# Kernel optimization log

Measured on AMD Instinct MI355X. Metric: run time of the kernel, lower is better.

The kernel has to match this reference:

```python
import jax, jax.numpy as jnp
import numpy as np

B, S, D, H = 2, 2048, 1024, 16
HD = D // H  # head dim = 64


def setup_inputs() -> dict:
    key = jax.random.key(0)
    k0, k1, k2 = jax.random.split(key, 3)
    x = jax.random.normal(k0, (B, S, D), dtype=jnp.float32)
    # fused QKV projection: nn.Linear(D, 3D) -> weight [3D, D], bias [3D]
    Wqkv_w = jax.random.normal(k1, (3 * D, D), dtype=jnp.float32) * (1.0 / np.sqrt(D))
    Wqkv_b = jnp.zeros((3 * D,), dtype=jnp.float32)
    out_w = jax.random.normal(k2, (D, D), dtype=jnp.float32) * (1.0 / np.sqrt(D))
    out_b = jnp.zeros((D,), dtype=jnp.float32)
    # ALiBi-like additive bias, shape [1, H, 1, S] (broadcasts over queries)
    slopes = 2.0 ** (-8.0 * jnp.arange(1, H + 1, dtype=jnp.float32) / H)  # [H]
    dist = (S - 1) - jnp.arange(S, dtype=jnp.float32)                      # [S]
    attn_bias = (-slopes[:, None] * dist[None, :]).reshape(1, H, 1, S)
    # key padding mask: second sequence is padded by 256 tokens at the end
    lengths = jnp.array([S, S - 256])
    attention_mask = jnp.arange(S)[None, :] < lengths[:, None]             # [B, S] bool
    return {"x": x, "Wqkv_w": Wqkv_w, "Wqkv_b": Wqkv_b, "out_w": out_w,
            "out_b": out_b, "attn_bias": attn_bias, "attention_mask": attention_mask}


def reference(x, Wqkv_w, Wqkv_b, out_w, out_b, attn_bias, attention_mask):
    b, s, d = x.shape
    # fused QKV projection, then chunk into q, k, v along feature dim
    qkv = jnp.einsum('bsd,ed->bse', x, Wqkv_w) + Wqkv_b  # [b, s, 3d]
    q, k, v = jnp.split(qkv, 3, axis=-1)
    # b s (h hd) -> b h s hd
    q = q.reshape(b, s, H, HD).transpose(0, 2, 1, 3)
    k = k.reshape(b, s, H, HD).transpose(0, 2, 1, 3)
    v = v.reshape(b, s, H, HD).transpose(0, 2, 1, 3)
    softmax_scale = 1.0 / np.sqrt(HD)
    aw = jnp.einsum('bhqe,bhke->bhqk', q, k) * softmax_scale  # [b, H, s, s]
    aw = aw + attn_bias  # attn_bias broadcasts [1,H,1,s] -> [b,H,s,s]
    min_val = jnp.finfo(aw.dtype).min
    # key padding mask: mask positions where attention_mask is False
    aw = jnp.where(attention_mask[:, None, None, :], aw, min_val)
    # causal mask (is_causal=True, s_q == s_k)
    causal = jnp.tril(jnp.ones((s, s), dtype=bool))
    aw = jnp.where(causal[None, None, :, :], aw, min_val)
    p = jax.nn.softmax(aw, axis=-1)
    out = jnp.einsum('bhqk,bhke->bhqe', p, v)  # [b, H, s, HD]
    out = out.transpose(0, 2, 1, 3).reshape(b, s, d)
    return jnp.einsum('bsd,ed->bse', out, out_w) + out_b
```

## Files before the change

kernel.cpp:

```cpp
#include <hip/hip_runtime.h>
#include <hip/hip_bf16.h>
#include <stdint.h>

typedef __attribute__((ext_vector_type(8))) short s16x8;
typedef __attribute__((ext_vector_type(8))) unsigned short u16x8;
typedef __attribute__((ext_vector_type(4))) float f32x4;

#define SEQ 2048
#define LOG2E 1.44269504088896f

__device__ __forceinline__ unsigned short f2b(float x) {
  union { __hip_bfloat16 h; unsigned short u; } cv;
  cv.h = __float2bfloat16(x);
  return cv.u;
}

__device__ __forceinline__ float exp2fast(float x) {
  float r;
  asm("v_exp_f32 %0, %1" : "=v"(r) : "v"(x));
  return r;
}

__device__ __forceinline__ void gload16(const void* g, void* l) {
  __builtin_amdgcn_global_load_lds(
      (const __attribute__((address_space(1))) void*)g,
      (__attribute__((address_space(3))) void*)l, 16, 0, 0);
}

__global__ void cvt_all(const float* __restrict__ x, const float* __restrict__ wq,
                        const float* __restrict__ ow, const float* __restrict__ abias,
                        const void* __restrict__ maskp,
                        __hip_bfloat16* __restrict__ xb, __hip_bfloat16* __restrict__ wqb,
                        __hip_bfloat16* __restrict__ owb, float* __restrict__ biasm) {
  const int i = blockIdx.x * 256 + threadIdx.x;
  if (i >= 2097152) {
    const int j = i - 2097152;
    const int b = j >> 15, h = (j >> 11) & 15, kv = j & 2047;
    const int* mi = (const int*)maskp;
    const unsigned char* mb = (const unsigned char*)maskp;
    const bool int_fmt = (mi[0] == 0 || mi[0] == 1);
    const bool ok = int_fmt ? (mi[b * SEQ + kv] != 0) : (mb[b * SEQ + kv] != 0);
    biasm[j] = ok ? abias[h * SEQ + kv] * LOG2E : -1e30f;
    return;
  }
  const float* src;
  __hip_bfloat16* dst;
  int off;
  if (i < 1048576) { src = x; dst = xb; off = i; }
  else if (i < 1835008) { src = wq; dst = wqb; off = i - 1048576; }
  else { src = ow; dst = owb; off = i - 1835008; }
  float4 v = reinterpret_cast<const float4*>(src)[off];
  ushort4 o;
  o.x = f2b(v.x); o.y = f2b(v.y); o.z = f2b(v.z); o.w = f2b(v.w);
  const int offs = off ^ ((((unsigned)off >> 8) & 3) << 1);
  reinterpret_cast<ushort4*>(dst)[offs] = o;
}

template <int MODE, int BM>
__global__ __launch_bounds__(256) void gemm_bt(
    const __hip_bfloat16* __restrict__ A, const __hip_bfloat16* __restrict__ B,
    const float* __restrict__ bias, void* __restrict__ Cout,
    __hip_bfloat16* __restrict__ Vt, int M, int N, int K) {
  constexpr int MR = BM / 32;
  __shared__ __align__(16) __hip_bfloat16 As[2][BM * 32];
  __shared__ __align__(16) __hip_bfloat16 Bs[2][128 * 32];
  const int tid = threadIdx.x;
  const int lane = tid & 63;
  const int w = tid >> 6;
  const int wr = w >> 1, wc = w & 1;
  const int rowg = blockIdx.x * BM;
  const int colg = blockIdx.y * 128;
  const int lr = lane & 15;
  const int lk = (((lane >> 4) ^ (lr & 3)) * 8);
  f32x4 acc[MR][4];
#pragma unroll
  for (int m = 0; m < MR; ++m)
#pragma unroll
    for (int n = 0; n < 4; ++n) acc[m][n] = (f32x4){0.f, 0.f, 0.f, 0.f};
#define GSTAGE(KT, C)                                                            \
  {                                                                              \
    _Pragma("unroll") for (int r = 0; r < BM / 64; ++r) {                        \
      const int idx = r * 256 + tid;                                             \
      gload16(A + (size_t)(rowg + (idx >> 2)) * K + (KT) + (idx & 3) * 8,        \
              &As[C][0] + idx * 8);                                              \
    }                                                                            \
    _Pragma("unroll") for (int r = 0; r < 2; ++r) {                              \
      const int idx = r * 256 + tid;                                             \
      gload16(B + (size_t)(colg + (idx >> 2)) * K + (KT) + (idx & 3) * 8,        \
              &Bs[C][0] + idx * 8);                                              \
    }                                                                            \
  }
  GSTAGE(0, 0);
  __syncthreads();
  int cur = 0;
  for (int kt = 0; kt < K; kt += 32) {
    if (kt + 32 < K) GSTAGE(kt + 32, cur ^ 1);
    s16x8 af[MR], bfr[4];
#pragma unroll
    for (int m = 0; m < MR; ++m)
      af[m] = *reinterpret_cast<const s16x8*>(&As[cur][0] +
                                              (wr * (BM / 2) + m * 16 + lr) * 32 + lk);
#pragma unroll
    for (int n = 0; n < 4; ++n)
      bfr[n] = *reinterpret_cast<const s16x8*>(&Bs[cur][0] +
                                               (wc * 64 + n * 16 + lr) * 32 + lk);
#pragma unroll
    for (int m = 0; m < MR; ++m)
#pragma unroll
      for (int n = 0; n < 4; ++n)
        acc[m][n] = __builtin_amdgcn_mfma_f32_16x16x32_bf16(af[m], bfr[n], acc[m][n], 0, 0, 0);
    __syncthreads();
    cur ^= 1;
  }
#undef GSTAGE
  const int r0l = (lane >> 4) * 4;
  float bvn[4];
#pragma unroll
  for (int n = 0; n < 4; ++n) bvn[n] = bias[colg + wc * 64 + n * 16 + lr];
#pragma unroll
  for (int m = 0; m < MR; ++m) {
#pragma unroll
    for (int n = 0; n < 4; ++n) {
      const int col = colg + wc * 64 + n * 16 + lr;
      const int row0 = rowg + wr * (BM / 2) + m * 16 + r0l;
      const float bv = bvn[n];
      if (MODE == 0) {
        __hip_bfloat16* qkb = (__hip_bfloat16*)Cout;
        if (col < 1024) {
#pragma unroll
          for (int j = 0; j < 4; ++j)
            qkb[(size_t)(row0 + j) * 2048 + col] = __float2bfloat16(acc[m][n][j] + bv);
        } else if (col < 2048) {
          const int dd = col & 63;
          const int base = col - dd;
#pragma unroll
          for (int j = 0; j < 4; ++j) {
            const int s = row0 + j;
            qkb[(size_t)s * 2048 + base + (dd ^ ((s & 7) << 3))] =
                __float2bfloat16(acc[m][n][j] + bv);
          }
        } else {
          const int c2 = col - 2048;
          const int dd = c2 & 63;
          const int bb = row0 >> 11;
          const int s0 = (row0 & 2047) ^ ((dd & 7) << 3);
          ushort4 pk;
          unsigned short* pp = (unsigned short*)&pk;
#pragma unroll
          for (int j = 0; j < 4; ++j) pp[j] = f2b(acc[m][n][j] + bv);
          *reinterpret_cast<ushort4*>(
              Vt + ((size_t)(bb * 16 + (c2 >> 6)) * 64 + dd) * 2048 + s0) = pk;
        }
      } else {
        float* o = (float*)Cout;
#pragma unroll
        for (int j = 0; j < 4; ++j)
          o[(size_t)(row0 + j) * N + col] = acc[m][n][j] + bv;
      }
    }
  }
}

__device__ __forceinline__ void attn_tile(
    const char* Ks, const char* Vs, char* pw, const float* bmb,
    s16x8 aq0, s16x8 aq1, int lane, int kv0, int q_abs, bool causal,
    int rd0, int rd1, const int* pwo,
    float m_r, float& l_r, f32x4* oa) {
  const int g = lane >> 4;
  const float SCALE2 = 0.125f * LOG2E;
  f32x4 bvp[4];
#pragma unroll
  for (int n = 0; n < 4; ++n) {
    bvp[n] = *reinterpret_cast<const f32x4*>(bmb + kv0 + n * 16 + g * 4);
#pragma unroll
    for (int j = 0; j < 4; ++j) bvp[n][j] -= m_r;
  }
  f32x4 sf[4];
  __builtin_amdgcn_s_setprio(1);
#pragma unroll
  for (int n = 0; n < 4; ++n) {
    s16x8 ak0 = *reinterpret_cast<const s16x8*>(Ks + rd0 + n * 2048);
    s16x8 ak1 = *reinterpret_cast<const s16x8*>(Ks + rd1 + n * 2048);
    f32x4 z = (f32x4){0.f, 0.f, 0.f, 0.f};
    z = __builtin_amdgcn_mfma_f32_16x16x32_bf16(ak0, aq0, z, 0, 0, 0);
    z = __builtin_amdgcn_mfma_f32_16x16x32_bf16(ak1, aq1, z, 0, 0, 0);
    sf[n] = z;
  }
  __builtin_amdgcn_s_setprio(0);
#pragma unroll
  for (int n = 0; n < 4; ++n)
#pragma unroll
    for (int j = 0; j < 4; ++j) sf[n][j] = fmaf(sf[n][j], SCALE2, bvp[n][j]);
  if (causal) {
    const int kvb = kv0 + g * 4;
#pragma unroll
    for (int n = 0; n < 4; ++n)
#pragma unroll
      for (int j = 0; j < 4; ++j)
        if (kvb + n * 16 + j > q_abs) sf[n][j] = -1e30f;
  }
  float ps[4];
#pragma unroll
  for (int n = 0; n < 4; ++n) {
#pragma unroll
    for (int j = 0; j < 4; ++j) sf[n][j] = exp2fast(sf[n][j]);
    ps[n] = (sf[n][0] + sf[n][1]) + (sf[n][2] + sf[n][3]);
  }
  l_r += (ps[0] + ps[1]) + (ps[2] + ps[3]);
  s16x8 bva[4], bvb[4];
#pragma unroll
  for (int d = 0; d < 4; ++d) {
    bva[d] = *reinterpret_cast<const s16x8*>(Vs + rd0 + d * 2048);
    bvb[d] = *reinterpret_cast<const s16x8*>(Vs + rd1 + d * 2048);
  }
#pragma unroll
  for (int n = 0; n < 4; ++n) {
    union { ushort4 u; uint2 v; } pk;
    pk.u.x = f2b(sf[n][0]); pk.u.y = f2b(sf[n][1]);
    pk.u.z = f2b(sf[n][2]); pk.u.w = f2b(sf[n][3]);
    *reinterpret_cast<uint2*>(pw + pwo[n]) = pk.v;
  }
  s16x8 pa0 = *reinterpret_cast<const s16x8*>(pw + rd0);
  s16x8 pa1 = *reinterpret_cast<const s16x8*>(pw + rd1);
  __builtin_amdgcn_s_setprio(1);
#pragma unroll
  for (int d = 0; d < 4; ++d) {
    oa[d] = __builtin_amdgcn_mfma_f32_16x16x32_bf16(pa0, bva[d], oa[d], 0, 0, 0);
    oa[d] = __builtin_amdgcn_mfma_f32_16x16x32_bf16(pa1, bvb[d], oa[d], 0, 0, 0);
  }
  __builtin_amdgcn_s_setprio(0);
}

__global__ __launch_bounds__(512, 4) void attn_fwd6(
    const __hip_bfloat16* __restrict__ qk, const __hip_bfloat16* __restrict__ Vt,
    const float* __restrict__ biasm, __hip_bfloat16* __restrict__ O) {
  __shared__ __align__(16) char KV[2][2][2][8192];
  __shared__ __align__(16) char Ps[8][2048];
  const int tid = threadIdx.x;
  const int lane = tid & 63;
  const int w = tid >> 6;
  const int wsub = w & 3;
  const int z = w >> 2;
  const int bid = blockIdx.x;
  const int qt = 31 - (bid >> 5);
  const int bh = bid & 31;
  const int b = bh >> 4, h = bh & 15;
  const int row0 = qt * 64 + wsub * 16;
  const int lr = lane & 15;
  const int g = lane >> 4;
  const int NTit = (qt >> 1) + 1;
  const int xm = (lr & 7) << 4;
  const int lkB = g * 16;
  const int rd0 = lr * 128 + (lkB ^ xm);
  const int rd1 = lr * 128 + ((64 + lkB) ^ xm);
  const int pwo[4] = {lr * 128 + ((g * 8) ^ xm),       lr * 128 + ((32 + g * 8) ^ xm),
                      lr * 128 + ((64 + g * 8) ^ xm),  lr * 128 + ((96 + g * 8) ^ xm)};
  const __hip_bfloat16* qptr =
      qk + (size_t)(b * SEQ + row0 + lr) * 2048 + h * 64 + g * 8;
  const s16x8 aq0 = *reinterpret_cast<const s16x8*>(qptr);
  const s16x8 aq1 = *reinterpret_cast<const s16x8*>(qptr + 32);
  const int q_abs = row0 + lr;
  const float* bmb = biasm + (size_t)bh * 2048;
  float mb = bmb[q_abs];
  if (mb < -1e29f) {
    int lo = 0, hi = q_abs;
    while (lo < hi) {
      const int mid = (lo + hi + 1) >> 1;
      if (bmb[mid] < -1e29f) hi = mid - 1; else lo = mid;
    }
    mb = bmb[lo];
  }
  const float m_r = mb + 12.0f;
  float l_r = 0.f;
  f32x4 oa[4];
#pragma unroll
  for (int d = 0; d < 4; ++d) oa[d] = (f32x4){0.f, 0.f, 0.f, 0.f};
  const int r_ = tid >> 3;
  const int c16 = tid & 7;
  const __hip_bfloat16* kb = qk + ((size_t)b * SEQ + r_) * 2048 + 1024 + h * 64 + c16 * 8;
  const __hip_bfloat16* vb = Vt + ((size_t)bh * 64 + r_) * 2048 + c16 * 8;
#define ISSUE(T, C)                                                     \
  {                                                                     \
    const int tE_ = 2 * (T);                                            \
    const int tO_ = (2 * (T) + 1 <= qt) ? (2 * (T) + 1) : qt;           \
    gload16(kb + (size_t)(tE_ * 64) * 2048, KV[0][C][0] + tid * 16);    \
    gload16(kb + (size_t)(tO_ * 64) * 2048, KV[1][C][0] + tid * 16);    \
    gload16(vb + tE_ * 64, KV[0][C][1] + tid * 16);                     \
    gload16(vb + tO_ * 64, KV[1][C][1] + tid * 16);                     \
  }
  ISSUE(0, 0);
  __syncthreads();
  int cur = 0;
  for (int t = 0; t < NTit; ++t) {
    if (t + 1 < NTit) ISSUE(t + 1, cur ^ 1);
    const int tz = 2 * t + z;
    if (tz <= qt)
      attn_tile(KV[z][cur][0], KV[z][cur][1], Ps[w], bmb, aq0, aq1, lane,
                tz * 64, q_abs, tz == qt, rd0, rd1, pwo, m_r, l_r, oa);
    __syncthreads();
    cur ^= 1;
  }
#undef ISSUE
  l_r += __shfl_xor(l_r, 16);
  l_r += __shfl_xor(l_r, 32);
  float* mlbuf = (float*)&KV[0][0][0][0];
  if (z == 1) {
    float* mo = (float*)(&Ps[0][0] + wsub * 4096);
#pragma unroll
    for (int d = 0; d < 4; ++d)
#pragma unroll
      for (int j = 0; j < 4; ++j)
        mo[(g * 4 + j) * 64 + d * 16 + lr] = oa[d][j];
    if (lane < 16) {
      mlbuf[wsub * 32 + lr] = m_r;
      mlbuf[wsub * 32 + 16 + lr] = l_r;
    }
  }
  __syncthreads();
  if (z == 0) {
    const float mB = mlbuf[wsub * 32 + lr];
    const float lB = mlbuf[wsub * 32 + 16 + lr];
    const float mS = fmaxf(m_r, mB);
    const float fA = exp2fast(m_r - mS);
    const float fB = exp2fast(mB - mS);
    const float linv = 1.0f / (l_r * fA + lB * fB);
    float fAj[4], fBj[4], lij[4];
#pragma unroll
    for (int j = 0; j < 4; ++j) {
      fAj[j] = __shfl(fA, g * 4 + j);
      fBj[j] = __shfl(fB, g * 4 + j);
      lij[j] = __shfl(linv, g * 4 + j);
    }
    const float* mo = (const float*)(&Ps[0][0] + wsub * 4096);
#pragma unroll
    for (int d = 0; d < 4; ++d)
#pragma unroll
      for (int j = 0; j < 4; ++j) {
        const float v =
            (oa[d][j] * fAj[j] + mo[(g * 4 + j) * 64 + d * 16 + lr] * fBj[j]) * lij[j];
        O[(size_t)(b * SEQ + row0 + g * 4 + j) * 1024 +
          ((h * 64 + d * 16 + lr) ^ (j << 3))] = __float2bfloat16(v);
      }
  }
}

extern "C" void kernel_launch(void* const* d_in, const int* in_sizes, int n_in,
                              void* d_out, int out_size, void* d_ws, size_t ws_size,
                              hipStream_t stream) {
  const float* x     = (const float*)d_in[0];
  const float* wqkv  = (const float*)d_in[1];
  const float* bqkv  = (const float*)d_in[2];
  const float* wout  = (const float*)d_in[3];
  const float* bout  = (const float*)d_in[4];
  const float* abias = (const float*)d_in[5];
  const void*  mask  = d_in[6];

  __hip_bfloat16* ws  = (__hip_bfloat16*)d_ws;
  __hip_bfloat16* xb  = ws;
  __hip_bfloat16* wqb = ws + 4194304;
  __hip_bfloat16* owb = ws + 7340032;
  __hip_bfloat16* qkb = ws + 8388608;
  __hip_bfloat16* vtb = ws + 16777216;
  float*          bmf = (float*)(ws + 20971520);
  __hip_bfloat16* aob = xb;

  cvt_all<<<8448, 256, 0, stream>>>(x, wqkv, wout, abias, mask, xb, wqb, owb, bmf);
  gemm_bt<0, 128><<<dim3(32, 24), 256, 0, stream>>>(xb, wqb, bqkv, (void*)qkb, vtb,
                                                    4096, 3072, 1024);
  attn_fwd6<<<1024, 512, 0, stream>>>(qkb, vtb, bmf, aob);
  gemm_bt<1, 64><<<dim3(64, 8), 256, 0, stream>>>(aob, owb, bout, d_out,
                                                  (__hip_bfloat16*)nullptr, 4096, 1024, 1024);
}
```

Baseline: 107.2 us.

## Keep softmax probabilities in registers by permuting K rows to match MFMA layout

Permutes which K rows each lane reads, and the matching bias and causal-mask indices, so the QK^T MFMA output already sits in the A-operand layout of the PV MFMA. The probabilities are then packed with v_cvt_pk_bf16_f32 straight into registers instead of going through an LDS write and read-back. This removes the per-wave Ps shared buffer, which lowers LDS use and may raise occupancy. The K swizzle in the QKV projection epilogue is changed to match the new read pattern, and the merge scratch now reuses the KV buffer, which needs care to avoid correctness or bank-conflict problems.

```diff
diff --git a/kernel.cpp b/kernel.cpp
--- a/kernel.cpp
+++ b/kernel.cpp
@@ -18,6 +18,12 @@
 __device__ __forceinline__ float exp2fast(float x) {
   float r;
   asm("v_exp_f32 %0, %1" : "=v"(r) : "v"(x));
+  return r;
+}
+
+__device__ __forceinline__ unsigned int cvtpk(float lo, float hi) {
+  unsigned int r;
+  asm("v_cvt_pk_bf16_f32 %0, %1, %2" : "=v"(r) : "v"(lo), "v"(hi));
   return r;
 }
 
@@ -136,7 +142,8 @@
 #pragma unroll
           for (int j = 0; j < 4; ++j) {
             const int s = row0 + j;
-            qkb[(size_t)s * 2048 + base + (dd ^ ((s & 7) << 3))] =
+            const int fs = (s & 3) | ((s & 8) >> 1);
+            qkb[(size_t)s * 2048 + base + (dd ^ (fs << 3))] =
                 __float2bfloat16(acc[m][n][j] + bv);
           }
         } else {
@@ -162,16 +169,17 @@
 }
 
 __device__ __forceinline__ void attn_tile(
-    const char* Ks, const char* Vs, char* pw, const float* bmb,
+    const char* Ks, const char* Vs, const float* bmb,
     s16x8 aq0, s16x8 aq1, int lane, int kv0, int q_abs, bool causal,
-    int rd0, int rd1, const int* pwo,
+    int rdK0, int rdK1, int rdV0, int rdV1,
     float m_r, float& l_r, f32x4* oa) {
   const int g = lane >> 4;
   const float SCALE2 = 0.125f * LOG2E;
   f32x4 bvp[4];
 #pragma unroll
   for (int n = 0; n < 4; ++n) {
-    bvp[n] = *reinterpret_cast<const f32x4*>(bmb + kv0 + n * 16 + g * 4);
+    bvp[n] = *reinterpret_cast<const f32x4*>(bmb + kv0 + (n >> 1) * 32 +
+                                             (n & 1) * 4 + g * 8);
 #pragma unroll
     for (int j = 0; j < 4; ++j) bvp[n][j] -= m_r;
   }
@@ -179,8 +187,9 @@
   __builtin_amdgcn_s_setprio(1);
 #pragma unroll
   for (int n = 0; n < 4; ++n) {
-    s16x8 ak0 = *reinterpret_cast<const s16x8*>(Ks + rd0 + n * 2048);
-    s16x8 ak1 = *reinterpret_cast<const s16x8*>(Ks + rd1 + n * 2048);
+    const int off = (n & 1) * 512 + (n >> 1) * 4096;
+    s16x8 ak0 = *reinterpret_cast<const s16x8*>(Ks + rdK0 + off);
+    s16x8 ak1 = *reinterpret_cast<const s16x8*>(Ks + rdK1 + off);
     f32x4 z = (f32x4){0.f, 0.f, 0.f, 0.f};
     z = __builtin_amdgcn_mfma_f32_16x16x32_bf16(ak0, aq0, z, 0, 0, 0);
     z = __builtin_amdgcn_mfma_f32_16x16x32_bf16(ak1, aq1, z, 0, 0, 0);
@@ -192,12 +201,13 @@
 #pragma unroll
     for (int j = 0; j < 4; ++j) sf[n][j] = fmaf(sf[n][j], SCALE2, bvp[n][j]);
   if (causal) {
-    const int kvb = kv0 + g * 4;
-#pragma unroll
-    for (int n = 0; n < 4; ++n)
+#pragma unroll
+    for (int n = 0; n < 4; ++n) {
+      const int kvb = kv0 + (n >> 1) * 32 + (n & 1) * 4 + g * 8;
 #pragma unroll
       for (int j = 0; j < 4; ++j)
-        if (kvb + n * 16 + j > q_abs) sf[n][j] = -1e30f;
+        if (kvb + j > q_abs) sf[n][j] = -1e30f;
+    }
   }
   float ps[4];
 #pragma unroll
@@ -210,23 +220,23 @@
   s16x8 bva[4], bvb[4];
 #pragma unroll
   for (int d = 0; d < 4; ++d) {
-    bva[d] = *reinterpret_cast<const s16x8*>(Vs + rd0 + d * 2048);
-    bvb[d] = *reinterpret_cast<const s16x8*>(Vs + rd1 + d * 2048);
-  }
-#pragma unroll
-  for (int n = 0; n < 4; ++n) {
-    union { ushort4 u; uint2 v; } pk;
-    pk.u.x = f2b(sf[n][0]); pk.u.y = f2b(sf[n][1]);
-    pk.u.z = f2b(sf[n][2]); pk.u.w = f2b(sf[n][3]);
-    *reinterpret_cast<uint2*>(pw + pwo[n]) = pk.v;
-  }
-  s16x8 pa0 = *reinterpret_cast<const s16x8*>(pw + rd0);
-  s16x8 pa1 = *reinterpret_cast<const s16x8*>(pw + rd1);
+    bva[d] = *reinterpret_cast<const s16x8*>(Vs + rdV0 + d * 2048);
+    bvb[d] = *reinterpret_cast<const s16x8*>(Vs + rdV1 + d * 2048);
+  }
+  union { unsigned int d[4]; s16x8 v; } p0, p1;
+  p0.d[0] = cvtpk(sf[0][0], sf[0][1]);
+  p0.d[1] = cvtpk(sf[0][2], sf[0][3]);
+  p0.d[2] = cvtpk(sf[1][0], sf[1][1]);
+  p0.d[3] = cvtpk(sf[1][2], sf[1][3]);
+  p1.d[0] = cvtpk(sf[2][0], sf[2][1]);
+  p1.d[1] = cvtpk(sf[2][2], sf[2][3]);
+  p1.d[2] = cvtpk(sf[3][0], sf[3][1]);
+  p1.d[3] = cvtpk(sf[3][2], sf[3][3]);
   __builtin_amdgcn_s_setprio(1);
 #pragma unroll
   for (int d = 0; d < 4; ++d) {
-    oa[d] = __builtin_amdgcn_mfma_f32_16x16x32_bf16(pa0, bva[d], oa[d], 0, 0, 0);
-    oa[d] = __builtin_amdgcn_mfma_f32_16x16x32_bf16(pa1, bvb[d], oa[d], 0, 0, 0);
+    oa[d] = __builtin_amdgcn_mfma_f32_16x16x32_bf16(p0.v, bva[d], oa[d], 0, 0, 0);
+    oa[d] = __builtin_amdgcn_mfma_f32_16x16x32_bf16(p1.v, bvb[d], oa[d], 0, 0, 0);
   }
   __builtin_amdgcn_s_setprio(0);
 }
@@ -235,7 +245,6 @@
     const __hip_bfloat16* __restrict__ qk, const __hip_bfloat16* __restrict__ Vt,
     const float* __restrict__ biasm, __hip_bfloat16* __restrict__ O) {
   __shared__ __align__(16) char KV[2][2][2][8192];
-  __shared__ __align__(16) char Ps[8][2048];
   const int tid = threadIdx.x;
   const int lane = tid & 63;
   const int w = tid >> 6;
@@ -250,11 +259,10 @@
   const int g = lane >> 4;
   const int NTit = (qt >> 1) + 1;
   const int xm = (lr & 7) << 4;
-  const int lkB = g * 16;
-  const int rd0 = lr * 128 + (lkB ^ xm);
-  const int rd1 = lr * 128 + ((64 + lkB) ^ xm);
-  const int pwo[4] = {lr * 128 + ((g * 8) ^ xm),       lr * 128 + ((32 + g * 8) ^ xm),
-                      lr * 128 + ((64 + g * 8) ^ xm),  lr * 128 + ((96 + g * 8) ^ xm)};
+  const int rdK0 = ((lr >> 2) * 8 + (lr & 3)) * 128 + ((g * 16) ^ xm);
+  const int rdK1 = rdK0 ^ 64;
+  const int rdV0 = lr * 128 + ((g * 16) ^ xm);
+  const int rdV1 = rdV0 ^ 64;
   const __hip_bfloat16* qptr =
       qk + (size_t)(b * SEQ + row0 + lr) * 2048 + h * 64 + g * 8;
   const s16x8 aq0 = *reinterpret_cast<const s16x8*>(qptr);
@@ -295,8 +303,8 @@
     if (t + 1 < NTit) ISSUE(t + 1, cur ^ 1);
     const int tz = 2 * t + z;
     if (tz <= qt)
-      attn_tile(KV[z][cur][0], KV[z][cur][1], Ps[w], bmb, aq0, aq1, lane,
-                tz * 64, q_abs, tz == qt, rd0, rd1, pwo, m_r, l_r, oa);
+      attn_tile(KV[z][cur][0], KV[z][cur][1], bmb, aq0, aq1, lane,
+                tz * 64, q_abs, tz == qt, rdK0, rdK1, rdV0, rdV1, m_r, l_r, oa);
     __syncthreads();
     cur ^= 1;
   }
@@ -304,8 +312,9 @@
   l_r += __shfl_xor(l_r, 16);
   l_r += __shfl_xor(l_r, 32);
   float* mlbuf = (float*)&KV[0][0][0][0];
+  float* moarea = (float*)&KV[1][0][0][0];
   if (z == 1) {
-    float* mo = (float*)(&Ps[0][0] + wsub * 4096);
+    float* mo = moarea + wsub * 1024;
 #pragma unroll
     for (int d = 0; d < 4; ++d)
 #pragma unroll
@@ -331,7 +340,7 @@
       fBj[j] = __shfl(fB, g * 4 + j);
       lij[j] = __shfl(linv, g * 4 + j);
     }
-    const float* mo = (const float*)(&Ps[0][0] + wsub * 4096);
+    const float* mo = moarea + wsub * 1024;
 #pragma unroll
     for (int d = 0; d < 4; ++d)
 #pragma unroll
```

Result: no change. 105.4 us (-1.7%).
